# Kernel optimization log

Hardware: AMD Instinct MI355X
Metric: run time of the kernel (lower is better)

## Reference

```python
import jax, jax.numpy as jnp
import numpy as np

B, C_IN, C_OUT = 32, 64, 128
K_SIZE, STRIDE, PAD, H = 3, 1, 1, 56
H_OUT = (H + 2 * PAD - K_SIZE) // STRIDE + 1


def setup_inputs() -> dict:
    key = jax.random.key(0)
    kx, kw = jax.random.split(key)
    x = jax.random.normal(kx, (B, C_IN, H, H), dtype=jnp.float32)
    # kaiming_uniform-ish init for K of shape [kh, kw, C_in, C_out]
    fan_in = K_SIZE * C_IN * C_OUT  # torch fan_in for this layout (dim1 * receptive field)
    bound = np.sqrt(6.0 / fan_in).astype(np.float32)
    K = jax.random.uniform(kw, (K_SIZE, K_SIZE, C_IN, C_OUT), dtype=jnp.float32,
                           minval=-bound, maxval=bound)
    return {"x": x, "K": K}


def reference(x, K):
    # Faithful to the torch code INCLUDING its mismatched flatten orders:
    #   patch flattened as (C_in, kh, kw); K flattened as (kh, kw, C_in).
    xp = jnp.pad(x, ((0, 0), (0, 0), (PAD, PAD), (PAD, PAD)))
    end = (H_OUT - 1) * STRIDE + 1
    # patches[b, c, di, dj, i, j] = xp[b, c, i*stride+di, j*stride+dj]
    rows = []
    for di in range(K_SIZE):
        cols = []
        for dj in range(K_SIZE):
            cols.append(xp[:, :, di:di + end:STRIDE, dj:dj + end:STRIDE])  # [B,C,Ho,Wo]
        rows.append(jnp.stack(cols, axis=2))  # [B,C,kw,Ho,Wo]
    patches = jnp.stack(rows, axis=2)  # [B, C, kh, kw, Ho, Wo]
    # flatten patch in (C, kh, kw) order -> [B, Ho, Wo, C*kh*kw]
    p = patches.transpose(0, 4, 5, 1, 2, 3).reshape(B, H_OUT, H_OUT, -1)
    # K flattened in (kh, kw, C) order, exactly as K.view(-1, out_channels)
    Kf = K.reshape(-1, C_OUT)  # [kh*kw*C_in, C_out]
    out = p @ Kf  # [B, Ho, Wo, C_out]
    return out.transpose(0, 3, 1, 2)  # [B, C_out, Ho, Wo]
```

## Files before the change

kernel.cpp:

```cpp
#include <hip/hip_runtime.h>
#include <hip/hip_bf16.h>
#include <stdint.h>


#define B_   32
#define CIN  64
#define COUT 128
#define H_   56
#define HP   58
#define F_   576

typedef __attribute__((ext_vector_type(8))) short bf16x8;
typedef __attribute__((ext_vector_type(4))) float f32x4;

#define XP_ELEMS (B_*HP*HP*CIN)
#define XP_SLACK 4096
#define XP_TOTAL (XP_ELEMS + XP_SLACK)
#define WG_ELEMS (COUT*F_)
#define WS_NEEDED ((size_t)(XP_TOTAL + WG_ELEMS) * 2)

#define NROW   (B_*HP)
#define NWBLK  (WG_ELEMS/256)

#define A_ALLOC 45568
#define LDS_TOT (A_ALLOC + 3*8192)

__global__ __launch_bounds__(256) void prep_all(const float* __restrict__ x,
                                                const float* __restrict__ K,
                                                __hip_bfloat16* __restrict__ xpT,
                                                __hip_bfloat16* __restrict__ WgT) {
  const int id = blockIdx.x;
  const int t  = threadIdx.x;

  if (id > NROW) {
    int n = (id - (NROW + 1))*256 + t;
    int co = n / F_, g = n % F_;
    int di = g / 192, dj = (g % 192) / 64, c = g & 63;
    int f  = c*9 + di*3 + dj;
    int kh = f / 192, kw = (f % 192) / 64, cc = f & 63;
    WgT[n] = __float2bfloat16(K[(((size_t)kh*3 + kw)*CIN + cc)*COUT + co]);
    return;
  }
  if (id == NROW) {
    bf16x8 z = (bf16x8)0;
    for (int idx = t; idx < XP_SLACK/8; idx += 256)
      ((bf16x8*)(xpT + XP_ELEMS))[idx] = z;
    return;
  }

  const int b = id / HP, h = id % HP;
  __hip_bfloat16* orow = xpT + (size_t)(b*HP + h) * HP * CIN;
  if (h == 0 || h == HP-1) {
    bf16x8 z = (bf16x8)0;
    for (int idx = t; idx < HP*CIN/8; idx += 256) ((bf16x8*)orow)[idx] = z;
    return;
  }
  __shared__ __align__(16) float scr[CIN*64];
  const float* xrow = x + ((size_t)(b*CIN)*H_ + (h-1)) * H_;
  for (int idx = t; idx < CIN*14; idx += 256) {
    int c = idx / 14, w4 = idx % 14;
    f32x4 v = *(const f32x4*)(xrow + (size_t)c*(H_*H_) + w4*4);
    *(f32x4*)&scr[c*64 + ((w4 + (c >> 3)) & 15)*4] = v;
  }
  __syncthreads();
  for (int idx = t; idx < HP*8; idx += 256) {
    int wp = idx >> 3, cg = (idx & 7) * 8;
    __align__(16) __hip_bfloat16 tmp[8];
    if (wp == 0 || wp == HP-1) {
#pragma unroll
      for (int k2 = 0; k2 < 8; ++k2) tmp[k2] = __float2bfloat16(0.f);
    } else {
      int w = wp - 1, sl = w >> 2, off = w & 3;
#pragma unroll
      for (int k2 = 0; k2 < 8; ++k2) {
        int c = cg + k2;
        tmp[k2] = __float2bfloat16(scr[c*64 + ((sl + (c >> 3)) & 15)*4 + off]);
      }
    }
    *(bf16x8*)(orow + (size_t)wp*CIN + cg) = *(const bf16x8*)tmp;
  }
}

__global__ __launch_bounds__(256, 2) void conv_mfma(
    const __hip_bfloat16* __restrict__ xpT,
    const __hip_bfloat16* __restrict__ WgT,
    float* __restrict__ out) {
  __shared__ __align__(16) char lds[LDS_TOT];
  const int t    = threadIdx.x;
  const int wave = t >> 6;
  const int l    = t & 63;
  const int lr   = l & 15, lq = l >> 4;

  const int bid = blockIdx.x;
  const int swz = (bid & 7) * 56 + (bid >> 3);
  const int bb  = swz / 14;
  const int i0  = (swz % 14) * 4;

  f32x4 acc[4][8];
#pragma unroll
  for (int mi = 0; mi < 4; ++mi)
#pragma unroll
    for (int ni = 0; ni < 8; ++ni) acc[mi][ni] = (f32x4)0.f;

  const char* xb    = (const char*)xpT + (size_t)(bb*HP + i0) * HP * CIN * 2;
  const char* wbase = (const char*)WgT;

#pragma unroll
  for (int s = 0; s < 11; ++s) {
    int o = s*4096 + t*16;
    int m = o >> 7;
    const char* src = xb + ((o & ~127) | ((o & 127) ^ ((m & 7) << 4)));
    __builtin_amdgcn_global_load_lds(
        (const __attribute__((address_space(1))) void*)src,
        (__attribute__((address_space(3))) void*)(lds + s*4096 + wave*1024),
        16, 0, 0);
  }

  int bsrc[2];
#pragma unroll
  for (int s = 0; s < 2; ++s) {
    int f  = s*256 + t;
    int ll = f & 63;
    int co = ((f >> 6)*16) + (ll & 15);
    bsrc[s] = co*1152 + ((ll >> 4)*16);
  }

  auto stageBh = [&](int hc, int buf) {
    const char* wg = wbase + hc*64;
    char* Bb = lds + A_ALLOC + buf*8192;
#pragma unroll
    for (int s = 0; s < 2; ++s) {
      __builtin_amdgcn_global_load_lds(
          (const __attribute__((address_space(1))) void*)(wg + bsrc[s]),
          (__attribute__((address_space(3))) void*)(Bb + s*4096 + wave*1024),
          16, 0, 0);
    }
  };

  stageBh(0, 0);
  stageBh(1, 1);
  asm volatile("s_waitcnt vmcnt(2)" ::: "memory");
  __builtin_amdgcn_s_barrier();

#pragma unroll
  for (int hc = 0; hc < 18; ++hc) {
    if (hc + 2 < 18) stageBh(hc + 2, (hc + 2) % 3);
    const char* Bb = lds + A_ALLOC + (hc % 3)*8192;
    const int kg  = hc*32;
    const int di  = kg / 192;
    const int rem = kg - di*192;
    bf16x8 a[4], bq[8];
#pragma unroll
    for (int mi = 0; mi < 4; ++mi) {
      int r   = (wave + di)*HP + mi*16 + lr;
      int tot = r*128 + rem*2 + lq*16;
      int adr = (tot & ~127) | ((tot & 127) ^ (((tot >> 7) & 7) << 4));
      a[mi] = *(const bf16x8*)(lds + adr);
    }
#pragma unroll
    for (int ni = 0; ni < 8; ++ni)
      bq[ni] = *(const bf16x8*)(Bb + (ni*64 + l)*16);
    __builtin_amdgcn_s_setprio(1);
#pragma unroll
    for (int mi = 0; mi < 4; ++mi)
#pragma unroll
      for (int ni = 0; ni < 8; ++ni)
        acc[mi][ni] = __builtin_amdgcn_mfma_f32_16x16x32_bf16(
            a[mi], bq[ni], acc[mi][ni], 0, 0, 0);
    __builtin_amdgcn_s_setprio(0);
    if (hc < 16) {
      asm volatile("s_waitcnt vmcnt(2)" ::: "memory");
      __builtin_amdgcn_s_barrier();
    } else if (hc == 16) {
      asm volatile("s_waitcnt vmcnt(0)" ::: "memory");
      __builtin_amdgcn_s_barrier();
    }
  }

  const int i = i0 + wave;
#pragma unroll
  for (int mi = 0; mi < 4; ++mi) {
    int j0 = mi*16 + lq*4;
    if (j0 < H_) {
#pragma unroll
      for (int ni = 0; ni < 8; ++ni) {
        int co = ni*16 + lr;
        float* dst = out + (((size_t)(bb*COUT + co))*H_ + i)*H_ + j0;
        *(f32x4*)dst = acc[mi][ni];
      }
    }
  }
}

__global__ __launch_bounds__(256) void conv_naive(const float* __restrict__ x,
                                                  const float* __restrict__ K,
                                                  float* __restrict__ out) {
  int idx = blockIdx.x*256 + threadIdx.x;
  const int total = B_*COUT*H_*H_;
  if (idx >= total) return;
  int j = idx % H_, i = (idx / H_) % H_, co = (idx / (H_*H_)) % COUT, b = idx / (H_*H_*COUT);
  float s = 0.f;
  for (int c = 0; c < CIN; ++c)
    for (int di = 0; di < 3; ++di) {
      int ii = i + di - 1;
      if (ii < 0 || ii >= H_) continue;
      for (int dj = 0; dj < 3; ++dj) {
        int jj = j + dj - 1;
        if (jj < 0 || jj >= H_) continue;
        int f = c*9 + di*3 + dj;
        int kh = f / 192, kw = (f % 192) / 64, cc = f & 63;
        s += x[(((size_t)b*CIN + c)*H_ + ii)*H_ + jj] *
             K[(((size_t)kh*3 + kw)*CIN + cc)*COUT + co];
      }
    }
  out[idx] = s;
}

extern "C" void kernel_launch(void* const* d_in, const int* in_sizes, int n_in,
                              void* d_out, int out_size, void* d_ws, size_t ws_size,
                              hipStream_t stream) {
  const float* x = (const float*)d_in[0];
  const float* K = (const float*)d_in[1];
  float* out = (float*)d_out;
  if (ws_size >= WS_NEEDED) {
    __hip_bfloat16* xpT = (__hip_bfloat16*)d_ws;
    __hip_bfloat16* WgT = xpT + XP_TOTAL;
    prep_all<<<NROW + 1 + NWBLK, 256, 0, stream>>>(x, K, xpT, WgT);
    conv_mfma<<<B_*14, 256, 0, stream>>>(xpT, WgT, out);
  } else {
    conv_naive<<<(B_*COUT*H_*H_ + 255)/256, 256, 0, stream>>>(x, K, out);
  }
}
```

Measured before the change: 39.71 us.

## Deepen weight staging to three slices and register-prefetch next B fragments

Weight slices are now staged three ahead in the LDS ring instead of two. The next slice's B fragments are read from LDS into a second register set before the current MFMA block runs, so the barrier and LDS reads overlap with matrix math instead of following it. The issue of the next global-to-LDS load moves to after the MFMAs. This costs about 32 extra VGPRs for the double-buffered fragments, which could hurt occupancy at two workgroups per CU or cause spills.

New measurement: 39.55 us. No clear change (-0.4%).

```diff
diff --git a/kernel.cpp b/kernel.cpp
--- a/kernel.cpp
+++ b/kernel.cpp
@@ -125,9 +125,9 @@
     bsrc[s] = co*1152 + ((ll >> 4)*16);
   }
 
-  auto stageBh = [&](int hc, int buf) {
+  auto stageBh = [&](int hc) {
     const char* wg = wbase + hc*64;
-    char* Bb = lds + A_ALLOC + buf*8192;
+    char* Bb = lds + A_ALLOC + (hc % 3)*8192;
 #pragma unroll
     for (int s = 0; s < 2; ++s) {
       __builtin_amdgcn_global_load_lds(
@@ -137,19 +137,22 @@
     }
   };
 
-  stageBh(0, 0);
-  stageBh(1, 1);
-  asm volatile("s_waitcnt vmcnt(2)" ::: "memory");
+  stageBh(0); stageBh(1); stageBh(2);
+  asm volatile("s_waitcnt vmcnt(4)" ::: "memory");
   __builtin_amdgcn_s_barrier();
+  __builtin_amdgcn_sched_barrier(0);
+
+  bf16x8 bcur[8], bnxt[8];
+#pragma unroll
+  for (int ni = 0; ni < 8; ++ni)
+    bcur[ni] = *(const bf16x8*)(lds + A_ALLOC + (ni*64 + l)*16);
 
 #pragma unroll
   for (int hc = 0; hc < 18; ++hc) {
-    if (hc + 2 < 18) stageBh(hc + 2, (hc + 2) % 3);
-    const char* Bb = lds + A_ALLOC + (hc % 3)*8192;
     const int kg  = hc*32;
     const int di  = kg / 192;
     const int rem = kg - di*192;
-    bf16x8 a[4], bq[8];
+    bf16x8 a[4];
 #pragma unroll
     for (int mi = 0; mi < 4; ++mi) {
       int r   = (wave + di)*HP + mi*16 + lr;
@@ -157,24 +160,27 @@
       int adr = (tot & ~127) | ((tot & 127) ^ (((tot >> 7) & 7) << 4));
       a[mi] = *(const bf16x8*)(lds + adr);
     }
-#pragma unroll
-    for (int ni = 0; ni < 8; ++ni)
-      bq[ni] = *(const bf16x8*)(Bb + (ni*64 + l)*16);
+    if (hc < 17) {
+      if (hc == 16) asm volatile("s_waitcnt vmcnt(0)" ::: "memory");
+      else          asm volatile("s_waitcnt vmcnt(2)" ::: "memory");
+      __builtin_amdgcn_s_barrier();
+      __builtin_amdgcn_sched_barrier(0);
+      const char* Bn = lds + A_ALLOC + ((hc + 1) % 3)*8192;
+#pragma unroll
+      for (int ni = 0; ni < 8; ++ni)
+        bnxt[ni] = *(const bf16x8*)(Bn + (ni*64 + l)*16);
+    }
     __builtin_amdgcn_s_setprio(1);
 #pragma unroll
     for (int mi = 0; mi < 4; ++mi)
 #pragma unroll
       for (int ni = 0; ni < 8; ++ni)
         acc[mi][ni] = __builtin_amdgcn_mfma_f32_16x16x32_bf16(
-            a[mi], bq[ni], acc[mi][ni], 0, 0, 0);
+            a[mi], bcur[ni], acc[mi][ni], 0, 0, 0);
     __builtin_amdgcn_s_setprio(0);
-    if (hc < 16) {
-      asm volatile("s_waitcnt vmcnt(2)" ::: "memory");
-      __builtin_amdgcn_s_barrier();
-    } else if (hc == 16) {
-      asm volatile("s_waitcnt vmcnt(0)" ::: "memory");
-      __builtin_amdgcn_s_barrier();
-    }
+    if (hc + 3 < 18) stageBh(hc + 3);
+#pragma unroll
+    for (int ni = 0; ni < 8; ++ni) bcur[ni] = bnxt[ni];
   }
 
   const int i = i0 + wave;
```
